# Kernel tuning notes

Hardware: AMD Instinct MI355X
Metric: run time of the kernel (lower is better)

The kernel has to match this reference:

```python
import jax, jax.numpy as jnp
import numpy as np

B, C, N, K = 2, 64, 16384, 16
C_OUT = 64


def setup_inputs() -> dict:
    key = jax.random.key(0)
    k1, k2, k3, k4 = jax.random.split(key, 4)
    x = jax.random.normal(k1, (B, C, N), dtype=jnp.float32)
    edge_index = jax.random.randint(k2, (2, B, N, K), 0, N, dtype=jnp.int64)
    # 1x1 Conv2d params: weight [C_out, 3C], bias [C_out]
    W = jax.random.normal(k3, (C_OUT, 3 * C), dtype=jnp.float32) * (1.0 / np.sqrt(3 * C))
    b = jax.random.normal(k4, (C_OUT,), dtype=jnp.float32) * 0.01
    return {"x": x, "edge_index": edge_index, "W": W, "b": b}


def _gather_nodes(x, idx):
    # x: [B, C, N], idx: [B, N, K] -> [B, C, N, K]
    return jax.vmap(lambda xb, ib: xb[:, ib])(x, idx)


def reference(x, edge_index, W, b):
    # x: [B, C, N]; edge_index: [2, B, N, K]
    x_i = _gather_nodes(x, edge_index[1])          # center features  [B,C,N,K]
    x_j = _gather_nodes(x, edge_index[0])          # neighbor features [B,C,N,K]
    edge_features = x_j - x_i                      # [B,C,N,K]
    global_feature = jnp.mean(x, axis=2, keepdims=True)  # [B,C,1] global mean over nodes
    global_rep = jnp.broadcast_to(global_feature[..., None], x_i.shape)  # [B,C,N,K]
    combined = jnp.concatenate([x_i, edge_features, global_rep], axis=1)  # [B,3C,N,K]
    # BasicConv: 1x1 conv + ReLU (norm=None)
    out = jnp.einsum("bcnk,oc->bonk", combined, W) + b[None, :, None, None]
    out = jax.nn.relu(out)
    return jnp.max(out, axis=-1, keepdims=True)    # [B,C_out,N,1]
```

## Files before the change

kernel.cpp:

```cpp
#include <hip/hip_runtime.h>
#include <hip/hip_bf16.h>


#define NNODES 16384
#define NCH 64

typedef _Float16 half8 __attribute__((ext_vector_type(8)));

__global__ __launch_bounds__(256) void mean_kernel(const float* __restrict__ x,
                                                   float* __restrict__ g) {
  int row = blockIdx.x;
  const float4* x4 = (const float4*)(x + (size_t)row * NNODES);
  int t = threadIdx.x;
  float s = 0.f;
#pragma unroll
  for (int i = 0; i < 16; ++i) {
    float4 q = x4[t + i * 256];
    s += (q.x + q.y) + (q.z + q.w);
  }
#pragma unroll
  for (int off = 32; off > 0; off >>= 1) s += __shfl_down(s, off, 64);
  __shared__ float wsum[4];
  int lane = t & 63, wv = t >> 6;
  if (lane == 0) wsum[wv] = s;
  __syncthreads();
  if (t == 0) g[row] = (wsum[0] + wsum[1] + wsum[2] + wsum[3]) * (1.0f / 16384.0f);
}

__global__ __launch_bounds__(256) void uv_kernel(const float* __restrict__ x,
                                                 const float* __restrict__ W,
                                                 _Float16* __restrict__ u,
                                                 _Float16* __restrict__ v) {
  __shared__ float A[64][64];
  __shared__ float Bm[64][64];
  int t = threadIdx.x;
  {
    int o = t & 63, c0 = (t >> 6) * 16;
    const float* wr = W + o * 192;
#pragma unroll
    for (int i = 0; i < 16; ++i) {
      int c = c0 + i;
      float w1 = wr[c], w2 = wr[64 + c];
      A[c][o] = w1 - w2;
      Bm[c][o] = w2;
    }
  }
  __syncthreads();
  int lane = t & 63;
  int wv = __builtin_amdgcn_readfirstlane(t >> 6);
  int blk = blockIdx.x;
  int b = blk >> 9;
  int m0 = (blk & 511) * 32 + wv * 8;
  const float* xb = x + (size_t)b * (NCH * NNODES) + m0;
  float aU[8], aV[8];
#pragma unroll
  for (int i = 0; i < 8; ++i) { aU[i] = 0.f; aV[i] = 0.f; }
#pragma unroll 8
  for (int c = 0; c < 64; ++c) {
    float a = A[c][lane];
    float bb = Bm[c][lane];
    const float4* xr = (const float4*)(xb + (size_t)c * NNODES);
    float4 q0 = xr[0];
    float4 q1 = xr[1];
    aU[0] += a * q0.x; aV[0] += bb * q0.x;
    aU[1] += a * q0.y; aV[1] += bb * q0.y;
    aU[2] += a * q0.z; aV[2] += bb * q0.z;
    aU[3] += a * q0.w; aV[3] += bb * q0.w;
    aU[4] += a * q1.x; aV[4] += bb * q1.x;
    aU[5] += a * q1.y; aV[5] += bb * q1.y;
    aU[6] += a * q1.z; aV[6] += bb * q1.z;
    aU[7] += a * q1.w; aV[7] += bb * q1.w;
  }
  _Float16* ub = u + ((size_t)b * NNODES + m0) * NCH + lane;
  _Float16* vb = v + ((size_t)b * NNODES + m0) * NCH + lane;
#pragma unroll
  for (int i = 0; i < 8; ++i) {
    ub[i * NCH] = (_Float16)aU[i];
    vb[i * NCH] = (_Float16)aV[i];
  }
}

__global__ __launch_bounds__(256) void gather_kernel(const int* __restrict__ ei,
                                                     const _Float16* __restrict__ u,
                                                     const _Float16* __restrict__ v,
                                                     const float* __restrict__ W,
                                                     const float* __restrict__ bias,
                                                     const float* __restrict__ g,
                                                     float* __restrict__ out) {
  __shared__ float tile[64][33];
  __shared__ float pg[4][64];
  __shared__ float G_s[64];
  int t = threadIdx.x;
  int lane = t & 63;
  int wv = t >> 6;
  int blk = blockIdx.x;
  int xcd = blk & 7;
  int b = xcd >> 2;
  int nb = (blk >> 3) * 4 + (xcd & 3);
  int n0 = nb * 32;
  int q = lane >> 3;
  int r = lane & 7;
  const int* e0b = ei + (size_t)b * NNODES * 16;
  const int* e1b = ei + (size_t)(2 + b) * NNODES * 16;
  int f0 = (n0 + wv * 8) * 16 + q * 16 + r;
  int i0a = e0b[f0];
  int i0b = e0b[f0 + 8];
  int i1a = e1b[f0];
  int i1b = e1b[f0 + 8];
  {
    int o = t >> 2, cq = t & 3;
    const float4* wr = (const float4*)(W + o * 192 + 128 + cq * 16);
    const float4* gr = (const float4*)(g + b * 64 + cq * 16);
    float s = 0.f;
#pragma unroll
    for (int j = 0; j < 4; ++j) {
      float4 w = wr[j];
      float4 gg = gr[j];
      s += w.x * gg.x + w.y * gg.y + w.z * gg.z + w.w * gg.w;
    }
    pg[cq][o] = s;
  }
  __syncthreads();
  if (t < 64) G_s[t] = bias[t] + ((pg[0][t] + pg[1][t]) + (pg[2][t] + pg[3][t]));
  __syncthreads();
  const half8* u8 = (const half8*)(u + (size_t)b * NNODES * NCH) + r;
  const half8* v8 = (const half8*)(v + (size_t)b * NNODES * NCH) + r;
  half8 acc;
#pragma unroll
  for (int j = 0; j < 8; ++j) acc[j] = (_Float16)(-60000.0f);
#pragma unroll
  for (int k = 0; k < 16; ++k) {
    int src = (lane & 56) + (k & 7);
    int m1 = __shfl(k < 8 ? i1a : i1b, src, 64);
    int m0 = __shfl(k < 8 ? i0a : i0b, src, 64);
    half8 a = u8[(size_t)m1 * 8];
    half8 bb = v8[(size_t)m0 * 8];
    half8 s = a + bb;
    acc = __builtin_elementwise_max(acc, s);
  }
  int col = wv * 8 + q;
#pragma unroll
  for (int j = 0; j < 8; ++j) {
    tile[r * 8 + j][col] = fmaxf((float)acc[j] + G_s[r * 8 + j], 0.0f);
  }
  __syncthreads();
#pragma unroll
  for (int j = 0; j < 8; ++j) {
    int o = (t >> 5) + j * 8;
    int c2 = t & 31;
    out[((size_t)b * 64 + o) * NNODES + n0 + c2] = tile[o][c2];
  }
}

extern "C" void kernel_launch(void* const* d_in, const int* in_sizes, int n_in,
                              void* d_out, int out_size, void* d_ws, size_t ws_size,
                              hipStream_t stream) {
  const float* x = (const float*)d_in[0];
  const int* ei = (const int*)d_in[1];
  const float* W = (const float*)d_in[2];
  const float* bias = (const float*)d_in[3];
  float* out = (float*)d_out;

  char* ws = (char*)d_ws;
  _Float16* u = (_Float16*)ws;
  _Float16* v = (_Float16*)(ws + (size_t)4 * 1024 * 1024);
  float* g = (float*)(ws + (size_t)8 * 1024 * 1024);

  mean_kernel<<<128, 256, 0, stream>>>(x, g);
  uv_kernel<<<1024, 256, 0, stream>>>(x, W, u, v);
  gather_kernel<<<1024, 256, 0, stream>>>(ei, u, v, W, bias, g, out);
}
```

Measured before the change: 93.59 us.

## Fuse global mean reduction into uv kernel via slotted atomics

Removes the separate mean kernel and computes per-channel partial sums inside uv_kernel, accumulating them with atomics into 8 slot arrays keyed by block index mod 8 to spread contention. The gather kernel then sums the slots and scales to get the mean. A memset replaces the mean kernel launch. This saves one launch and one full read of x, but adds a memset launch, an extra sync and atomics.

```diff
diff --git a/kernel.cpp b/kernel.cpp
--- a/kernel.cpp
+++ b/kernel.cpp
@@ -7,32 +7,14 @@
 
 typedef _Float16 half8 __attribute__((ext_vector_type(8)));
 
-__global__ __launch_bounds__(256) void mean_kernel(const float* __restrict__ x,
-                                                   float* __restrict__ g) {
-  int row = blockIdx.x;
-  const float4* x4 = (const float4*)(x + (size_t)row * NNODES);
-  int t = threadIdx.x;
-  float s = 0.f;
-#pragma unroll
-  for (int i = 0; i < 16; ++i) {
-    float4 q = x4[t + i * 256];
-    s += (q.x + q.y) + (q.z + q.w);
-  }
-#pragma unroll
-  for (int off = 32; off > 0; off >>= 1) s += __shfl_down(s, off, 64);
-  __shared__ float wsum[4];
-  int lane = t & 63, wv = t >> 6;
-  if (lane == 0) wsum[wv] = s;
-  __syncthreads();
-  if (t == 0) g[row] = (wsum[0] + wsum[1] + wsum[2] + wsum[3]) * (1.0f / 16384.0f);
-}
-
 __global__ __launch_bounds__(256) void uv_kernel(const float* __restrict__ x,
                                                  const float* __restrict__ W,
                                                  _Float16* __restrict__ u,
-                                                 _Float16* __restrict__ v) {
+                                                 _Float16* __restrict__ v,
+                                                 float* __restrict__ g_slots) {
   __shared__ float A[64][64];
   __shared__ float Bm[64][64];
+  __shared__ float csum[4][64];
   int t = threadIdx.x;
   {
     int o = t & 63, c0 = (t >> 6) * 16;
@@ -50,7 +32,8 @@
   int wv = __builtin_amdgcn_readfirstlane(t >> 6);
   int blk = blockIdx.x;
   int b = blk >> 9;
-  int m0 = (blk & 511) * 32 + wv * 8;
+  int mb = (blk & 511) * 32;
+  int m0 = mb + wv * 8;
   const float* xb = x + (size_t)b * (NCH * NNODES) + m0;
   float aU[8], aV[8];
 #pragma unroll
@@ -78,6 +61,19 @@
     ub[i * NCH] = (_Float16)aU[i];
     vb[i * NCH] = (_Float16)aV[i];
   }
+  {
+    int c = t & 63, piece = t >> 6;
+    const float4* xr2 =
+        (const float4*)(x + (size_t)b * (NCH * NNODES) + (size_t)c * NNODES + mb + piece * 8);
+    float4 a0 = xr2[0];
+    float4 a1 = xr2[1];
+    csum[piece][c] = ((a0.x + a0.y) + (a0.z + a0.w)) + ((a1.x + a1.y) + (a1.z + a1.w));
+  }
+  __syncthreads();
+  if (t < 64) {
+    float s = (csum[0][t] + csum[1][t]) + (csum[2][t] + csum[3][t]);
+    atomicAdd(&g_slots[((blk & 7) << 7) + b * 64 + t], s);
+  }
 }
 
 __global__ __launch_bounds__(256) void gather_kernel(const int* __restrict__ ei,
@@ -85,9 +81,10 @@
                                                      const _Float16* __restrict__ v,
                                                      const float* __restrict__ W,
                                                      const float* __restrict__ bias,
-                                                     const float* __restrict__ g,
+                                                     const float* __restrict__ g_slots,
                                                      float* __restrict__ out) {
   __shared__ float tile[64][33];
+  __shared__ float gb[64];
   __shared__ float pg[4][64];
   __shared__ float G_s[64];
   int t = threadIdx.x;
@@ -107,10 +104,17 @@
   int i0b = e0b[f0 + 8];
   int i1a = e1b[f0];
   int i1b = e1b[f0 + 8];
+  if (t < 64) {
+    float s = 0.f;
+#pragma unroll
+    for (int sl = 0; sl < 8; ++sl) s += g_slots[sl * 128 + b * 64 + t];
+    gb[t] = s * (1.0f / 16384.0f);
+  }
+  __syncthreads();
   {
     int o = t >> 2, cq = t & 3;
     const float4* wr = (const float4*)(W + o * 192 + 128 + cq * 16);
-    const float4* gr = (const float4*)(g + b * 64 + cq * 16);
+    const float4* gr = (const float4*)(gb + cq * 16);
     float s = 0.f;
 #pragma unroll
     for (int j = 0; j < 4; ++j) {
@@ -164,9 +168,9 @@
   char* ws = (char*)d_ws;
   _Float16* u = (_Float16*)ws;
   _Float16* v = (_Float16*)(ws + (size_t)4 * 1024 * 1024);
-  float* g = (float*)(ws + (size_t)8 * 1024 * 1024);
+  float* g_slots = (float*)(ws + (size_t)8 * 1024 * 1024);
 
-  mean_kernel<<<128, 256, 0, stream>>>(x, g);
-  uv_kernel<<<1024, 256, 0, stream>>>(x, W, u, v);
-  gather_kernel<<<1024, 256, 0, stream>>>(ei, u, v, W, bias, g, out);
+  hipMemsetAsync(g_slots, 0, 8 * 128 * sizeof(float), stream);
+  uv_kernel<<<1024, 256, 0, stream>>>(x, W, u, v, g_slots);
+  gather_kernel<<<1024, 256, 0, stream>>>(ei, u, v, W, bias, g_slots, out);
 }
```

After: 92.63 us. Within noise of the previous version (-1.0%).
